# Kernel tuning notes

Measured on AMD Instinct MI355X. Metric: run time of the kernel, lower is better.

Reference implementation:

```python
import jax, jax.numpy as jnp
import numpy as np

N, F, H, C = 50000, 128, 4, 32  # nodes, in-features, heads, per-head dim
E = 800000
D = H * C  # concat output dim = 128


def _tconv(x, src, dst, ea, Wq, bq, Wk, bk, Wv, bv, We, Ws, bs):
    # PyG TransformerConv (concat=True, root_weight=True, beta=False, eval mode)
    n = x.shape[0]
    q = (x @ Wq + bq).reshape(n, H, C)
    k = (x @ Wk + bk).reshape(n, H, C)
    v = (x @ Wv + bv).reshape(n, H, C)
    e = (ea @ We).reshape(-1, H, C)            # edge embedding [E,H,C]
    kj = k[src] + e                            # gathered keys + edge emb
    alpha = jnp.einsum('ehc,ehc->eh', q[dst], kj) / jnp.sqrt(jnp.float32(C))
    amax = jax.ops.segment_max(alpha, dst, num_segments=n)
    ex = jnp.exp(alpha - amax[dst])
    denom = jax.ops.segment_sum(ex, dst, num_segments=n)
    w = ex / (denom[dst] + 1e-16)              # segment softmax over in-edges
    msg = (v[src] + e) * w[:, :, None]
    out = jax.ops.segment_sum(msg, dst, num_segments=n).reshape(n, D)
    return out + x @ Ws + bs                   # skip connection


def setup_inputs() -> dict:
    key = jax.random.key(0)
    ks = jax.random.split(key, 24)
    s = lambda i, shape, scale: jax.random.normal(ks[i], shape, dtype=jnp.float32) * scale
    inp = {
        'x': s(0, (N, F), 1.0),
        'edge_index': jax.random.randint(ks[1], (2, E), 0, N),
        'edge_attr': s(2, (E,), 1.0),
        # layer 1 (in = F)
        'Wq1': s(3, (F, D), 1.0 / np.sqrt(F)), 'bq1': jnp.zeros((D,), jnp.float32),
        'Wk1': s(4, (F, D), 1.0 / np.sqrt(F)), 'bk1': jnp.zeros((D,), jnp.float32),
        'Wv1': s(5, (F, D), 1.0 / np.sqrt(F)), 'bv1': jnp.zeros((D,), jnp.float32),
        'We1': s(6, (1, D), 1.0),
        'Ws1': s(7, (F, D), 1.0 / np.sqrt(F)), 'bs1': jnp.zeros((D,), jnp.float32),
        # layer 2 (in = D)
        'Wq2': s(8, (D, D), 1.0 / np.sqrt(D)), 'bq2': jnp.zeros((D,), jnp.float32),
        'Wk2': s(9, (D, D), 1.0 / np.sqrt(D)), 'bk2': jnp.zeros((D,), jnp.float32),
        'Wv2': s(10, (D, D), 1.0 / np.sqrt(D)), 'bv2': jnp.zeros((D,), jnp.float32),
        'We2': s(11, (1, D), 1.0),
        'Ws2': s(12, (D, D), 1.0 / np.sqrt(D)), 'bs2': jnp.zeros((D,), jnp.float32),
    }
    return inp


def reference(x, edge_index, edge_attr,
              Wq1, bq1, Wk1, bk1, Wv1, bv1, We1, Ws1, bs1,
              Wq2, bq2, Wk2, bk2, Wv2, bv2, We2, Ws2, bs2):
    src, dst = edge_index[0], edge_index[1]
    ea = edge_attr.reshape(-1, 1)
    h = _tconv(x, src, dst, ea, Wq1, bq1, Wk1, bk1, Wv1, bv1, We1, Ws1, bs1)
    h = jax.nn.relu(h)  # dropout is identity in eval mode
    h = _tconv(h, src, dst, ea, Wq2, bq2, Wk2, bk2, Wv2, bv2, We2, Ws2, bs2)
    return jax.nn.relu(h)
```

## Files before the change

### kernel.cpp

```cpp
#include <hip/hip_runtime.h>


#define TPB 256

typedef __attribute__((ext_vector_type(8))) short short8v;
typedef __attribute__((ext_vector_type(8))) unsigned short ushort8v;
typedef __attribute__((ext_vector_type(16))) float f32x16;

__device__ __forceinline__ unsigned short f2bf(float f) {
    unsigned u = __float_as_uint(f);
    u = (u + 0x7FFFu + ((u >> 16) & 1u)) >> 16;
    return (unsigned short)u;
}
__device__ __forceinline__ float bf2f(unsigned short s) {
    return __uint_as_float((unsigned)s << 16);
}
__device__ __forceinline__ float exp2_hw(float x) {
    float r;
    asm("v_exp_f32 %0, %1" : "=v"(r) : "v"(x));
    return r;
}

__global__ void __launch_bounds__(TPB) prep_cvt_k(
    const float* __restrict__ Wq1, const float* __restrict__ Wk1,
    const float* __restrict__ Wv1, const float* __restrict__ Ws1,
    const float* __restrict__ Wq2, const float* __restrict__ Wk2,
    const float* __restrict__ Wv2, const float* __restrict__ Ws2,
    unsigned short* __restrict__ pack,
    const float* __restrict__ x, unsigned short* __restrict__ xb, int n4)
{
    if (blockIdx.x < 512) {
        int i = blockIdx.x * TPB + threadIdx.x;
        int j = i & 7, lane = (i >> 3) & 63, t = (i >> 9) & 7, nc = (i >> 12) & 3, g = (i >> 14) & 7;
        const float* Wt[8] = {Wq1, Wk1, Wv1, Ws1, Wq2, Wk2, Wv2, Ws2};
        const float* W = Wt[g];
        int kk = t * 16 + (lane >> 5) * 8 + j;
        int nn = nc * 32 + (lane & 31);
        pack[i] = f2bf(W[kk * 128 + nn]);
    } else {
        int i = (blockIdx.x - 512) * TPB + threadIdx.x;
        if (i >= n4) return;
        float4 v = *(const float4*)(x + (size_t)i * 4);
        ushort4 o;
        o.x = f2bf(v.x); o.y = f2bf(v.y); o.z = f2bf(v.z); o.w = f2bf(v.w);
        *(ushort4*)(xb + (size_t)i * 4) = o;
    }
}

__global__ void __launch_bounds__(TPB) gemm_mfma_k(
    const unsigned short* __restrict__ A, int M,
    const unsigned short* __restrict__ pack,
    const float* __restrict__ bq, const float* __restrict__ bk,
    const float* __restrict__ bv, const float* __restrict__ bs,
    unsigned short* __restrict__ oq, unsigned short* __restrict__ okv,
    float* __restrict__ os)
{
    const int g = blockIdx.y;
    const int row0 = blockIdx.x * 128;
    const int wv = threadIdx.x >> 6;
    const int lane = threadIdx.x & 63;
    const int rbase = row0 + wv * 32;
    const int arow = rbase + (lane & 31);
    const int kh = (lane >> 5) * 8;

    const short8v z8 = {0, 0, 0, 0, 0, 0, 0, 0};
    short8v a[8];
    if (arow < M) {
        const unsigned short* Ap = A + (size_t)arow * 128 + kh;
#pragma unroll
        for (int t = 0; t < 8; ++t) a[t] = *(const short8v*)(Ap + t * 16);
    } else {
#pragma unroll
        for (int t = 0; t < 8; ++t) a[t] = z8;
    }

    f32x16 acc[4];
#pragma unroll
    for (int nc = 0; nc < 4; ++nc)
#pragma unroll
        for (int r = 0; r < 16; ++r) acc[nc][r] = 0.f;

    const unsigned short* bp = pack + (size_t)g * 16384;
#pragma unroll
    for (int nc = 0; nc < 4; ++nc) {
#pragma unroll
        for (int t = 0; t < 8; ++t) {
            short8v b = *(const short8v*)(bp + (nc * 8 + t) * 512 + lane * 8);
            acc[nc] = __builtin_amdgcn_mfma_f32_32x32x16_bf16(a[t], b, acc[nc], 0, 0, 0);
        }
    }

    const float* bias = g == 0 ? bq : (g == 1 ? bk : (g == 2 ? bv : bs));
    const int col = lane & 31;
    const int rb2 = rbase + 4 * (lane >> 5);
    if (g == 3) {
#pragma unroll
        for (int nc = 0; nc < 4; ++nc) {
            float bb = bias[nc * 32 + col];
#pragma unroll
            for (int r = 0; r < 16; ++r) {
                int row = rb2 + (r & 3) + 8 * (r >> 2);
                if (row < M) os[(size_t)row * 128 + nc * 32 + col] = acc[nc][r] + bb;
            }
        }
    } else {
        unsigned short* out = g == 0 ? oq : okv;
        const int stride = g == 0 ? 128 : 256;
        const int goff = g == 2 ? 128 : 0;
#pragma unroll
        for (int nc = 0; nc < 4; ++nc) {
            float bb = bias[nc * 32 + col];
#pragma unroll
            for (int r = 0; r < 16; ++r) {
                int row = rb2 + (r & 3) + 8 * (r >> 2);
                if (row < M)
                    out[(size_t)row * stride + goff + nc * 32 + col] = f2bf(acc[nc][r] + bb);
            }
        }
    }
}

__global__ void __launch_bounds__(TPB) hist_k(const int* __restrict__ dst,
                                              int* __restrict__ deg, int E)
{
    int e = blockIdx.x * TPB + threadIdx.x;
    if (e < E) atomicAdd(&deg[dst[e]], 1);
}

__global__ void __launch_bounds__(TPB) scan_a_k(const int* __restrict__ deg, int n,
                                                int* __restrict__ incl,
                                                int* __restrict__ bsum)
{
    __shared__ int ts[TPB];
    const int base = blockIdx.x * 1024;
    int vals[4], s = 0;
#pragma unroll
    for (int j = 0; j < 4; ++j) {
        int i = base + threadIdx.x * 4 + j;
        vals[j] = (i < n) ? deg[i] : 0;
        s += vals[j];
    }
    ts[threadIdx.x] = s;
    __syncthreads();
    for (int off = 1; off < TPB; off <<= 1) {
        int u = (threadIdx.x >= off) ? ts[threadIdx.x - off] : 0;
        __syncthreads();
        ts[threadIdx.x] += u;
        __syncthreads();
    }
    int run = ts[threadIdx.x] - s;
#pragma unroll
    for (int j = 0; j < 4; ++j) {
        run += vals[j];
        int i = base + threadIdx.x * 4 + j;
        if (i < n) incl[i] = run;
    }
    if (threadIdx.x == TPB - 1) bsum[blockIdx.x] = ts[TPB - 1];
}

__global__ void __launch_bounds__(TPB) scan_b_k(int* __restrict__ bsum, int nb)
{
    __shared__ int ts[TPB];
    int t = threadIdx.x;
    int v = (t < nb) ? bsum[t] : 0;
    ts[t] = v;
    __syncthreads();
    for (int off = 1; off < TPB; off <<= 1) {
        int u = (t >= off) ? ts[t - off] : 0;
        __syncthreads();
        ts[t] += u;
        __syncthreads();
    }
    if (t < nb) bsum[t] = ts[t] - v;
}

__global__ void __launch_bounds__(TPB) finalize_k(const int* __restrict__ incl,
                                                  const int* __restrict__ deg,
                                                  const int* __restrict__ bsum, int n,
                                                  int* __restrict__ row_ptr,
                                                  int* __restrict__ cursor)
{
    const int base = blockIdx.x * 1024;
    const int boff = bsum[blockIdx.x];
#pragma unroll
    for (int j = 0; j < 4; ++j) {
        int i = base + threadIdx.x * 4 + j;
        if (i < n) {
            int iv = incl[i] + boff;
            int st = iv - deg[i];
            row_ptr[i] = st;
            cursor[i] = st;
            if (i == n - 1) row_ptr[n] = iv;
        }
    }
}

__global__ void __launch_bounds__(TPB) scatter_k(
    const int* __restrict__ src, const int* __restrict__ dst,
    const float* __restrict__ ea, int* __restrict__ cursor,
    int2* __restrict__ csr_pair, int E)
{
    int e = blockIdx.x * TPB + threadIdx.x;
    if (e >= E) return;
    int pos = atomicAdd(&cursor[dst[e]], 1);
    csr_pair[pos] = make_int2(src[e], __float_as_int(ea[e]));
}

template <bool BF16OUT>
__global__ void __launch_bounds__(TPB) node_attn_k(
    const unsigned short* __restrict__ q, const unsigned short* __restrict__ kv,
    const float* __restrict__ skip, const float* __restrict__ We,
    const int* __restrict__ row_ptr, const int2* __restrict__ csr_pair,
    void* __restrict__ outp, int n)
{
    const int node = blockIdx.x * 16 + (threadIdx.x >> 4);
    if (node >= n) return;
    const int l16 = threadIdx.x & 15;
    const int c8 = l16 * 8;

    const float C2 = 0.17677669529663687f * 1.44269504088896f;

    float we8[8], qv[8];
    {
        float4 wlo = *(const float4*)(We + c8);
        float4 whi = *(const float4*)(We + c8 + 4);
        we8[0] = wlo.x; we8[1] = wlo.y; we8[2] = wlo.z; we8[3] = wlo.w;
        we8[4] = whi.x; we8[5] = whi.y; we8[6] = whi.z; we8[7] = whi.w;
        ushort8v qu = *(const ushort8v*)(q + (size_t)node * 128 + c8);
#pragma unroll
        for (int i = 0; i < 8; ++i) qv[i] = bf2f((unsigned short)qu[i]) * C2;
    }

    float qwe = 0.f;
#pragma unroll
    for (int i = 0; i < 8; ++i) qwe = fmaf(qv[i], we8[i], qwe);
    qwe += __shfl_xor(qwe, 1);
    qwe += __shfl_xor(qwe, 2);

    const int p0 = row_ptr[node], p1 = row_ptr[node + 1];

    float m = -3.4e38f, l = 0.f, sae = 0.f;
    float acc[8];
#pragma unroll
    for (int i = 0; i < 8; ++i) acc[i] = 0.f;

    for (int j = p0; j < p1; j += 4) {
        const int last = p1 - 1;
        int2 pr0 = csr_pair[j];
        int2 pr1 = csr_pair[min(j + 1, last)];
        int2 pr2 = csr_pair[min(j + 2, last)];
        int2 pr3 = csr_pair[min(j + 3, last)];
        const unsigned short* b0 = kv + (unsigned)pr0.x * 256u + c8;
        const unsigned short* b1 = kv + (unsigned)pr1.x * 256u + c8;
        const unsigned short* b2 = kv + (unsigned)pr2.x * 256u + c8;
        const unsigned short* b3 = kv + (unsigned)pr3.x * 256u + c8;
        ushort8v ku0 = *(const ushort8v*)b0;
        ushort8v ku1 = *(const ushort8v*)b1;
        ushort8v ku2 = *(const ushort8v*)b2;
        ushort8v ku3 = *(const ushort8v*)b3;
        ushort8v vu0 = *(const ushort8v*)(b0 + 128);
        ushort8v vu1 = *(const ushort8v*)(b1 + 128);
        ushort8v vu2 = *(const ushort8v*)(b2 + 128);
        ushort8v vu3 = *(const ushort8v*)(b3 + 128);

        float d0 = 0.f, d1 = 0.f, d2 = 0.f, d3 = 0.f;
#pragma unroll
        for (int i = 0; i < 8; ++i) {
            d0 = fmaf(bf2f((unsigned short)ku0[i]), qv[i], d0);
            d1 = fmaf(bf2f((unsigned short)ku1[i]), qv[i], d1);
            d2 = fmaf(bf2f((unsigned short)ku2[i]), qv[i], d2);
            d3 = fmaf(bf2f((unsigned short)ku3[i]), qv[i], d3);
        }
        d0 += __shfl_xor(d0, 1); d0 += __shfl_xor(d0, 2);
        d1 += __shfl_xor(d1, 1); d1 += __shfl_xor(d1, 2);
        d2 += __shfl_xor(d2, 1); d2 += __shfl_xor(d2, 2);
        d3 += __shfl_xor(d3, 1); d3 += __shfl_xor(d3, 2);

        float ea0 = __int_as_float(pr0.y), ea1 = __int_as_float(pr1.y);
        float ea2 = __int_as_float(pr2.y), ea3 = __int_as_float(pr3.y);
        float al0 = fmaf(ea0, qwe, d0);
        float al1 = (j + 1 < p1) ? fmaf(ea1, qwe, d1) : -3.4e38f;
        float al2 = (j + 2 < p1) ? fmaf(ea2, qwe, d2) : -3.4e38f;
        float al3 = (j + 3 < p1) ? fmaf(ea3, qwe, d3) : -3.4e38f;

        float mn = fmaxf(m, fmaxf(fmaxf(al0, al1), fmaxf(al2, al3)));
        float sc = exp2_hw(m - mn);
        float pe0 = exp2_hw(al0 - mn), pe1 = exp2_hw(al1 - mn);
        float pe2 = exp2_hw(al2 - mn), pe3 = exp2_hw(al3 - mn);

        l = fmaf(l, sc, (pe0 + pe1) + (pe2 + pe3));
        sae = fmaf(sae, sc, fmaf(pe3, ea3, fmaf(pe2, ea2, fmaf(pe1, ea1, pe0 * ea0))));
#pragma unroll
        for (int i = 0; i < 8; ++i) {
            float mv = fmaf(pe0, bf2f((unsigned short)vu0[i]),
                       fmaf(pe1, bf2f((unsigned short)vu1[i]),
                       fmaf(pe2, bf2f((unsigned short)vu2[i]),
                            pe3 * bf2f((unsigned short)vu3[i]))));
            acc[i] = fmaf(acc[i], sc, mv);
        }
        m = mn;
    }

    float inv = 1.f / (l + 1e-16f);
    float4 sklo = *(const float4*)(skip + (size_t)node * 128 + c8);
    float4 skhi = *(const float4*)(skip + (size_t)node * 128 + c8 + 4);
    float sk[8] = {sklo.x, sklo.y, sklo.z, sklo.w, skhi.x, skhi.y, skhi.z, skhi.w};
    float o[8];
#pragma unroll
    for (int i = 0; i < 8; ++i)
        o[i] = fmaxf(fmaf(fmaf(sae, we8[i], acc[i]), inv, sk[i]), 0.f);

    if (BF16OUT) {
        ushort8v ov;
#pragma unroll
        for (int i = 0; i < 8; ++i) ov[i] = f2bf(o[i]);
        *(ushort8v*)((unsigned short*)outp + (size_t)node * 128 + c8) = ov;
    } else {
        float* op = (float*)outp + (size_t)node * 128 + c8;
        *(float4*)op = make_float4(o[0], o[1], o[2], o[3]);
        *(float4*)(op + 4) = make_float4(o[4], o[5], o[6], o[7]);
    }
}

extern "C" void kernel_launch(void* const* d_in, const int* in_sizes, int n_in,
                              void* d_out, int out_size, void* d_ws, size_t ws_size,
                              hipStream_t stream)
{
    const float* x   = (const float*)d_in[0];
    const int*   ei  = (const int*)d_in[1];
    const float* ea  = (const float*)d_in[2];
    const float* Wq1 = (const float*)d_in[3];  const float* bq1 = (const float*)d_in[4];
    const float* Wk1 = (const float*)d_in[5];  const float* bk1 = (const float*)d_in[6];
    const float* Wv1 = (const float*)d_in[7];  const float* bv1 = (const float*)d_in[8];
    const float* We1 = (const float*)d_in[9];
    const float* Ws1 = (const float*)d_in[10]; const float* bs1 = (const float*)d_in[11];
    const float* Wq2 = (const float*)d_in[12]; const float* bq2 = (const float*)d_in[13];
    const float* Wk2 = (const float*)d_in[14]; const float* bk2 = (const float*)d_in[15];
    const float* Wv2 = (const float*)d_in[16]; const float* bv2 = (const float*)d_in[17];
    const float* We2 = (const float*)d_in[18];
    const float* Ws2 = (const float*)d_in[19]; const float* bs2 = (const float*)d_in[20];

    const int N = in_sizes[0] / 128;
    const int E = in_sizes[1] / 2;
    const int* src = ei;
    const int* dst = ei + E;
    float* outf = (float*)d_out;

    unsigned short* q  = (unsigned short*)d_ws;
    unsigned short* kv = q + (size_t)N * 128;
    float*          s  = (float*)(kv + (size_t)N * 256);
    unsigned short* xb = (unsigned short*)(s + (size_t)N * 128);
    unsigned short* pk = xb + (size_t)N * 128;
    int*   row_ptr = (int*)(pk + 131072);
    int*   deg     = row_ptr + (N + 1);
    int*   incl    = deg + N;
    int*   cursor  = incl + N;
    int*   bsum    = cursor + N;
    int2*  csr_pair = (int2*)(((uintptr_t)(bsum + 256) + 7) & ~(uintptr_t)7);

    const int gE   = (E + TPB - 1) / TPB;
    const int nb   = (N + 1023) / 1024;
    const int gN16 = (N + 15) / 16;
    const int n4   = N * 128 / 4;
    const int gPC  = 512 + (n4 + TPB - 1) / TPB;
    const int gG   = (N + 127) / 128;
    const dim3 gGd(gG, 4);

    hipMemsetAsync(deg, 0, (size_t)N * sizeof(int), stream);
    hist_k<<<gE, TPB, 0, stream>>>(dst, deg, E);
    scan_a_k<<<nb, TPB, 0, stream>>>(deg, N, incl, bsum);
    scan_b_k<<<1, TPB, 0, stream>>>(bsum, nb);
    finalize_k<<<nb, TPB, 0, stream>>>(incl, deg, bsum, N, row_ptr, cursor);
    scatter_k<<<gE, TPB, 0, stream>>>(src, dst, ea, cursor, csr_pair, E);

    prep_cvt_k<<<gPC, TPB, 0, stream>>>(Wq1, Wk1, Wv1, Ws1, Wq2, Wk2, Wv2, Ws2,
                                        pk, x, xb, n4);

    gemm_mfma_k<<<gGd, TPB, 0, stream>>>(xb, N, pk, bq1, bk1, bv1, bs1, q, kv, s);
    node_attn_k<true><<<gN16, TPB, 0, stream>>>(q, kv, s, We1, row_ptr, csr_pair,
                                                xb, N);
    gemm_mfma_k<<<gGd, TPB, 0, stream>>>(xb, N, pk + 65536, bq2, bk2, bv2, bs2,
                                         q, kv, s);
    node_attn_k<false><<<gN16, TPB, 0, stream>>>(q, kv, s, We2, row_ptr, csr_pair,
                                                 outf, N);
}
```

Baseline: 324.2 us.

## Sort nodes by degree and pack CSR entries into 32-bit words

Builds a degree histogram during the scan, prefix-sums it, and writes a permutation that orders nodes by descending degree. The attention kernels walk nodes in that order, so neighbouring 16-lane groups get similar edge counts and waste fewer lanes on divergent loop lengths. The CSR entry shrinks from an int2 to one 32-bit word: a 16-bit source index and a bf16 edge attribute. This halves CSR traffic in both layers, but it only works while N is at most 65536 and it lowers the precision of the edge attribute. It also adds heavily contended histogram atomics and an extra indirection through the permutation.

```diff
diff --git a/kernel.cpp b/kernel.cpp
--- a/kernel.cpp
+++ b/kernel.cpp
@@ -129,7 +129,8 @@
 
 __global__ void __launch_bounds__(TPB) scan_a_k(const int* __restrict__ deg, int n,
                                                 int* __restrict__ incl,
-                                                int* __restrict__ bsum)
+                                                int* __restrict__ bsum,
+                                                int* __restrict__ dhist)
 {
     __shared__ int ts[TPB];
     const int base = blockIdx.x * 1024;
@@ -139,6 +140,7 @@
         int i = base + threadIdx.x * 4 + j;
         vals[j] = (i < n) ? deg[i] : 0;
         s += vals[j];
+        if (i < n) atomicAdd(&dhist[min(vals[j], 1023)], 1);
     }
     ts[threadIdx.x] = s;
     __syncthreads();
@@ -158,7 +160,8 @@
     if (threadIdx.x == TPB - 1) bsum[blockIdx.x] = ts[TPB - 1];
 }
 
-__global__ void __launch_bounds__(TPB) scan_b_k(int* __restrict__ bsum, int nb)
+__global__ void __launch_bounds__(TPB) scan_b_k(int* __restrict__ bsum, int nb,
+                                                int* __restrict__ dhist)
 {
     __shared__ int ts[TPB];
     int t = threadIdx.x;
@@ -172,13 +175,39 @@
         __syncthreads();
     }
     if (t < nb) bsum[t] = ts[t] - v;
+    __syncthreads();
+
+    int vals[4], s = 0;
+#pragma unroll
+    for (int j = 0; j < 4; ++j) {
+        vals[j] = dhist[t * 4 + j];
+        s += vals[j];
+    }
+    __syncthreads();
+    ts[t] = s;
+    __syncthreads();
+    for (int off = 1; off < TPB; off <<= 1) {
+        int u = (t >= off) ? ts[t - off] : 0;
+        __syncthreads();
+        ts[t] += u;
+        __syncthreads();
+    }
+    int run = ts[t] - s;
+#pragma unroll
+    for (int j = 0; j < 4; ++j) {
+        run += vals[j];
+        dhist[t * 4 + j] = run;
+    }
 }
 
 __global__ void __launch_bounds__(TPB) finalize_k(const int* __restrict__ incl,
                                                   const int* __restrict__ deg,
                                                   const int* __restrict__ bsum, int n,
                                                   int* __restrict__ row_ptr,
-                                                  int* __restrict__ cursor)
+                                                  int* __restrict__ cursor,
+                                                  const int* __restrict__ dhist,
+                                                  int* __restrict__ dcur,
+                                                  int* __restrict__ perm)
 {
     const int base = blockIdx.x * 1024;
     const int boff = bsum[blockIdx.x];
@@ -186,11 +215,15 @@
     for (int j = 0; j < 4; ++j) {
         int i = base + threadIdx.x * 4 + j;
         if (i < n) {
+            int dg = deg[i];
             int iv = incl[i] + boff;
-            int st = iv - deg[i];
+            int st = iv - dg;
             row_ptr[i] = st;
             cursor[i] = st;
             if (i == n - 1) row_ptr[n] = iv;
+            int db = min(dg, 1023);
+            int pos = (n - dhist[db]) + atomicAdd(&dcur[db], 1);
+            perm[pos] = i;
         }
     }
 }
@@ -198,23 +231,25 @@
 __global__ void __launch_bounds__(TPB) scatter_k(
     const int* __restrict__ src, const int* __restrict__ dst,
     const float* __restrict__ ea, int* __restrict__ cursor,
-    int2* __restrict__ csr_pair, int E)
+    unsigned* __restrict__ csr_pack, int E)
 {
     int e = blockIdx.x * TPB + threadIdx.x;
     if (e >= E) return;
     int pos = atomicAdd(&cursor[dst[e]], 1);
-    csr_pair[pos] = make_int2(src[e], __float_as_int(ea[e]));
+    csr_pack[pos] = ((unsigned)f2bf(ea[e]) << 16) | (unsigned)src[e];
 }
 
 template <bool BF16OUT>
 __global__ void __launch_bounds__(TPB) node_attn_k(
     const unsigned short* __restrict__ q, const unsigned short* __restrict__ kv,
     const float* __restrict__ skip, const float* __restrict__ We,
-    const int* __restrict__ row_ptr, const int2* __restrict__ csr_pair,
+    const int* __restrict__ row_ptr, const unsigned* __restrict__ csr_pack,
+    const int* __restrict__ perm,
     void* __restrict__ outp, int n)
 {
-    const int node = blockIdx.x * 16 + (threadIdx.x >> 4);
-    if (node >= n) return;
+    const int slot = blockIdx.x * 16 + (threadIdx.x >> 4);
+    if (slot >= n) return;
+    const int node = perm[slot];
     const int l16 = threadIdx.x & 15;
     const int c8 = l16 * 8;
 
@@ -246,14 +281,14 @@
 
     for (int j = p0; j < p1; j += 4) {
         const int last = p1 - 1;
-        int2 pr0 = csr_pair[j];
-        int2 pr1 = csr_pair[min(j + 1, last)];
-        int2 pr2 = csr_pair[min(j + 2, last)];
-        int2 pr3 = csr_pair[min(j + 3, last)];
-        const unsigned short* b0 = kv + (unsigned)pr0.x * 256u + c8;
-        const unsigned short* b1 = kv + (unsigned)pr1.x * 256u + c8;
-        const unsigned short* b2 = kv + (unsigned)pr2.x * 256u + c8;
-        const unsigned short* b3 = kv + (unsigned)pr3.x * 256u + c8;
+        unsigned pr0 = csr_pack[j];
+        unsigned pr1 = csr_pack[min(j + 1, last)];
+        unsigned pr2 = csr_pack[min(j + 2, last)];
+        unsigned pr3 = csr_pack[min(j + 3, last)];
+        const unsigned short* b0 = kv + (pr0 & 0xFFFFu) * 256u + c8;
+        const unsigned short* b1 = kv + (pr1 & 0xFFFFu) * 256u + c8;
+        const unsigned short* b2 = kv + (pr2 & 0xFFFFu) * 256u + c8;
+        const unsigned short* b3 = kv + (pr3 & 0xFFFFu) * 256u + c8;
         ushort8v ku0 = *(const ushort8v*)b0;
         ushort8v ku1 = *(const ushort8v*)b1;
         ushort8v ku2 = *(const ushort8v*)b2;
@@ -276,8 +311,10 @@
         d2 += __shfl_xor(d2, 1); d2 += __shfl_xor(d2, 2);
         d3 += __shfl_xor(d3, 1); d3 += __shfl_xor(d3, 2);
 
-        float ea0 = __int_as_float(pr0.y), ea1 = __int_as_float(pr1.y);
-        float ea2 = __int_as_float(pr2.y), ea3 = __int_as_float(pr3.y);
+        float ea0 = bf2f((unsigned short)(pr0 >> 16));
+        float ea1 = bf2f((unsigned short)(pr1 >> 16));
+        float ea2 = bf2f((unsigned short)(pr2 >> 16));
+        float ea3 = bf2f((unsigned short)(pr3 >> 16));
         float al0 = fmaf(ea0, qwe, d0);
         float al1 = (j + 1 < p1) ? fmaf(ea1, qwe, d1) : -3.4e38f;
         float al2 = (j + 2 < p1) ? fmaf(ea2, qwe, d2) : -3.4e38f;
@@ -353,10 +390,13 @@
     unsigned short* pk = xb + (size_t)N * 128;
     int*   row_ptr = (int*)(pk + 131072);
     int*   deg     = row_ptr + (N + 1);
-    int*   incl    = deg + N;
+    int*   dhist   = deg + N;
+    int*   dcur    = dhist + 1024;
+    int*   incl    = dcur + 1024;
     int*   cursor  = incl + N;
     int*   bsum    = cursor + N;
-    int2*  csr_pair = (int2*)(((uintptr_t)(bsum + 256) + 7) & ~(uintptr_t)7);
+    int*   perm    = bsum + 256;
+    unsigned* csr_pack = (unsigned*)(perm + N);
 
     const int gE   = (E + TPB - 1) / TPB;
     const int nb   = (N + 1023) / 1024;
@@ -366,21 +406,22 @@
     const int gG   = (N + 127) / 128;
     const dim3 gGd(gG, 4);
 
-    hipMemsetAsync(deg, 0, (size_t)N * sizeof(int), stream);
+    hipMemsetAsync(deg, 0, (size_t)(N + 2048) * sizeof(int), stream);
     hist_k<<<gE, TPB, 0, stream>>>(dst, deg, E);
-    scan_a_k<<<nb, TPB, 0, stream>>>(deg, N, incl, bsum);
-    scan_b_k<<<1, TPB, 0, stream>>>(bsum, nb);
-    finalize_k<<<nb, TPB, 0, stream>>>(incl, deg, bsum, N, row_ptr, cursor);
-    scatter_k<<<gE, TPB, 0, stream>>>(src, dst, ea, cursor, csr_pair, E);
+    scan_a_k<<<nb, TPB, 0, stream>>>(deg, N, incl, bsum, dhist);
+    scan_b_k<<<1, TPB, 0, stream>>>(bsum, nb, dhist);
+    finalize_k<<<nb, TPB, 0, stream>>>(incl, deg, bsum, N, row_ptr, cursor,
+                                       dhist, dcur, perm);
+    scatter_k<<<gE, TPB, 0, stream>>>(src, dst, ea, cursor, csr_pack, E);
 
     prep_cvt_k<<<gPC, TPB, 0, stream>>>(Wq1, Wk1, Wv1, Ws1, Wq2, Wk2, Wv2, Ws2,
                                         pk, x, xb, n4);
 
     gemm_mfma_k<<<gGd, TPB, 0, stream>>>(xb, N, pk, bq1, bk1, bv1, bs1, q, kv, s);
-    node_attn_k<true><<<gN16, TPB, 0, stream>>>(q, kv, s, We1, row_ptr, csr_pair,
-                                                xb, N);
+    node_attn_k<true><<<gN16, TPB, 0, stream>>>(q, kv, s, We1, row_ptr, csr_pack,
+                                                perm, xb, N);
     gemm_mfma_k<<<gGd, TPB, 0, stream>>>(xb, N, pk + 65536, bq2, bk2, bv2, bs2,
                                          q, kv, s);
-    node_attn_k<false><<<gN16, TPB, 0, stream>>>(q, kv, s, We2, row_ptr, csr_pair,
-                                                 outf, N);
-}
+    node_attn_k<false><<<gN16, TPB, 0, stream>>>(q, kv, s, We2, row_ptr, csr_pack,
+                                                 perm, outf, N);
+}
```

Result: slower. 594.1 us (+83.3%).
